# Performance work log

Measured on AMD Instinct MI355X. Metric: run time of the kernel, lower is better.

## Reference

```python
import jax, jax.numpy as jnp
import numpy as np

B_, L_, D_, N_ = 2, 2048, 512, 64

def setup_inputs() -> dict:
    key = jax.random.key(0)
    ks = jax.random.split(key, 6)
    s = 1.0 / np.sqrt(D_)
    return {
        "x": jax.random.normal(ks[0], (B_, L_, D_), dtype=jnp.float32),
        "W1": jax.random.normal(ks[1], (D_, D_), dtype=jnp.float32) * s,
        "b1": jnp.zeros((D_,), dtype=jnp.float32),
        "W2": jax.random.normal(ks[2], (D_, N_), dtype=jnp.float32) * s,
        "b2": jnp.zeros((N_,), dtype=jnp.float32),
        "W3": jax.random.normal(ks[3], (D_, N_), dtype=jnp.float32) * s,
        "b3": jnp.zeros((N_,), dtype=jnp.float32),
        "A": jax.random.normal(ks[4], (D_, N_), dtype=jnp.float32) * (1.0 / np.sqrt(N_)),
    }

def reference(x, W1, b1, W2, b2, W3, b3, A):
    # Projections (faithful to fc2/fc3/fc1 in the torch module)
    B = x @ W2 + b2                                  # (b, l, n)
    C = x @ W3 + b3                                  # (b, l, n)
    delta = jax.nn.softplus(x @ W1 + b1)             # (b, l, d)
    # Discretization
    dB = jnp.einsum('bld,bln->bldn', delta, B)       # (b, l, d, n)
    dA = jnp.exp(jnp.einsum('bld,dn->bldn', delta, A))  # (b, l, d, n)
    # h is initialized to zeros in the original forward, so the dA*h term
    # contributes exactly zero; kept for faithfulness to the source math.
    h = dA * 0.0 + x[..., None] * dB                 # (b, l, d, n)
    y = jnp.einsum('bln,bldn->bld', C, h)            # (b, l, d)
    return y
```

## Files before the change

### kernel.cpp

```cpp
#include <hip/hip_runtime.h>
#include <math.h>

#define DDIM 512
#define MTOK 4096

typedef _Float16 f16;
typedef _Float16 f16x4 __attribute__((ext_vector_type(4)));
typedef _Float16 f16x8 __attribute__((ext_vector_type(8)));
typedef float f32x4 __attribute__((ext_vector_type(4)));

__device__ __forceinline__ float softplusf(float v) {
    return (v > 20.0f) ? v : log1pf(__expf(v));
}

__device__ __forceinline__ void async_load16(const void* g, void* l) {
    __builtin_amdgcn_global_load_lds(
        (const __attribute__((address_space(1))) void*)g,
        (__attribute__((address_space(3))) void*)l, 16, 0, 0);
}

__global__ __launch_bounds__(256) void prep_kernel(
    const float* __restrict__ x,  const float* __restrict__ W1,
    const float* __restrict__ W2, const float* __restrict__ W3,
    f16* __restrict__ xh, f16* __restrict__ w1t, f16* __restrict__ w23)
{
    const int tid = threadIdx.x;
    if (blockIdx.x < 2048) {
        size_t gid = ((size_t)blockIdx.x * 256 + tid) * 4;
        float4 v = *(const float4*)(x + gid);
        f16x4 h = {(f16)v.x, (f16)v.y, (f16)v.z, (f16)v.w};
        *(f16x4*)(xh + gid) = h;
        return;
    }
    __shared__ f16 lt[64][72];
    int b2 = blockIdx.x - 2048;
    const float* src; f16* dst; int srcRS;
    if (b2 < 64) {
        int kt = b2 >> 3, nt = b2 & 7;
        src = W1 + (size_t)(kt * 64) * DDIM + nt * 64; srcRS = DDIM;
        dst = w1t + (size_t)(nt * 64) * DDIM + kt * 64;
    } else if (b2 < 72) {
        int kt = b2 - 64;
        src = W2 + (size_t)(kt * 64) * 64; srcRS = 64;
        dst = w23 + kt * 64;
    } else {
        int kt = b2 - 72;
        src = W3 + (size_t)(kt * 64) * 64; srcRS = 64;
        dst = w23 + (size_t)64 * DDIM + kt * 64;
    }
    int r  = tid >> 2;
    int cg = tid & 3;
#pragma unroll
    for (int p = 0; p < 4; ++p) {
        float4 v = *(const float4*)(src + (size_t)r * srcRS + cg * 16 + p * 4);
        lt[cg * 16 + p * 4 + 0][r] = (f16)v.x;
        lt[cg * 16 + p * 4 + 1][r] = (f16)v.y;
        lt[cg * 16 + p * 4 + 2][r] = (f16)v.z;
        lt[cg * 16 + p * 4 + 3][r] = (f16)v.w;
    }
    __syncthreads();
    *(f16x8*)(dst + (size_t)r * DDIM + cg * 16)     = *(const f16x8*)&lt[r][cg * 16];
    *(f16x8*)(dst + (size_t)r * DDIM + cg * 16 + 8) = *(const f16x8*)&lt[r][cg * 16 + 8];
}

#define S_BUF 20480
__global__ __launch_bounds__(256) void s_kernel(
    const f16* __restrict__ xh, const f16* __restrict__ w23,
    const float* __restrict__ b2, const float* __restrict__ b3,
    float* __restrict__ s_out)
{
    __shared__ __align__(16) char smem[2 * S_BUF + 512];
    float* sred = (float*)(smem + 2 * S_BUF);

    const int tid  = threadIdx.x;
    const int wv   = tid >> 6;
    const int lane = tid & 63;
    const int q    = lane >> 4;
    const int l15  = lane & 15;
    const int tb   = blockIdx.x * 32;

    f32x4 acc[2][2];
#pragma unroll
    for (int m = 0; m < 2; ++m)
#pragma unroll
        for (int p = 0; p < 2; ++p) acc[m][p] = (f32x4){0.f, 0.f, 0.f, 0.f};

    auto issue = [&](int buf, int kc) {
#pragma unroll
        for (int j = 0; j < 5; ++j) {
            int id = wv * 5 + j;
            const f16* g; int off;
            if (id < 4) {
                int mt = id >> 1, kk = id & 1;
                g = xh + (size_t)(tb + mt * 16 + l15) * DDIM + kc + kk * 32 + q * 8;
                off = id * 1024;
            } else {
                int t = id - 4; int nt = t >> 1, kk = t & 1;
                g = w23 + (size_t)(nt * 16 + l15) * DDIM + kc + kk * 32 + q * 8;
                off = 4096 + t * 1024;
            }
            async_load16(g, smem + buf * S_BUF + off);
        }
    };

    issue(0, 0);
    for (int it = 0; it < 8; ++it) {
        __syncthreads();
        if (it + 1 < 8) issue((it + 1) & 1, (it + 1) * 64);
        const char* xb = smem + (it & 1) * S_BUF;
        const char* wb = xb + 4096;
#pragma unroll
        for (int kk = 0; kk < 2; ++kk) {
            f16x8 a0 = *(const f16x8*)(xb + (0 * 2 + kk) * 1024 + lane * 16);
            f16x8 a1 = *(const f16x8*)(xb + (1 * 2 + kk) * 1024 + lane * 16);
            f16x8 bB = *(const f16x8*)(wb + ((wv    ) * 2 + kk) * 1024 + lane * 16);
            f16x8 bC = *(const f16x8*)(wb + ((wv + 4) * 2 + kk) * 1024 + lane * 16);
            acc[0][0] = __builtin_amdgcn_mfma_f32_16x16x32_f16(a0, bB, acc[0][0], 0, 0, 0);
            acc[0][1] = __builtin_amdgcn_mfma_f32_16x16x32_f16(a0, bC, acc[0][1], 0, 0, 0);
            acc[1][0] = __builtin_amdgcn_mfma_f32_16x16x32_f16(a1, bB, acc[1][0], 0, 0, 0);
            acc[1][1] = __builtin_amdgcn_mfma_f32_16x16x32_f16(a1, bC, acc[1][1], 0, 0, 0);
        }
    }

    float b2v = b2[wv * 16 + l15];
    float b3v = b3[wv * 16 + l15];
#pragma unroll
    for (int m = 0; m < 2; ++m)
#pragma unroll
        for (int r = 0; r < 4; ++r) {
            float p = (acc[m][0][r] + b2v) * (acc[m][1][r] + b3v);
            p += __shfl_xor(p, 1); p += __shfl_xor(p, 2);
            p += __shfl_xor(p, 4); p += __shfl_xor(p, 8);
            if (l15 == 0) sred[wv * 32 + m * 16 + q * 4 + r] = p;
        }
    __syncthreads();
    if (tid < 32)
        s_out[tb + tid] = sred[tid] + sred[32 + tid] + sred[64 + tid] + sred[96 + tid];
}

#define Y_BUF 24576
__global__ __launch_bounds__(512) void y_kernel(
    const f16* __restrict__ xh, const f16* __restrict__ w1t,
    const float* __restrict__ b1, const float* __restrict__ s_in,
    float* __restrict__ y)
{
    __shared__ __align__(16) char smem[2 * Y_BUF];

    const int tid  = threadIdx.x;
    const int wv   = tid >> 6;
    const int lane = tid & 63;
    const int q    = lane >> 4;
    const int l15  = lane & 15;
    const int db   = blockIdx.x * 64;
    const int tb   = blockIdx.y * 128;

    f32x4 acc[4];
#pragma unroll
    for (int nt = 0; nt < 4; ++nt) acc[nt] = (f32x4){0.f, 0.f, 0.f, 0.f};

    auto issue = [&](int buf, int kc) {
#pragma unroll
        for (int j = 0; j < 3; ++j) {
            int id = wv * 3 + j;
            const f16* g; int off;
            if (id < 16) {
                int mt = id >> 1, kk = id & 1;
                g = xh + (size_t)(tb + mt * 16 + l15) * DDIM + kc + kk * 32 + q * 8;
                off = id * 1024;
            } else {
                int t = id - 16; int nt = t >> 1, kk = t & 1;
                g = w1t + (size_t)(db + nt * 16 + l15) * DDIM + kc + kk * 32 + q * 8;
                off = 16384 + t * 1024;
            }
            async_load16(g, smem + buf * Y_BUF + off);
        }
    };

    issue(0, 0);
    for (int it = 0; it < 8; ++it) {
        __syncthreads();
        if (it + 1 < 8) issue((it + 1) & 1, (it + 1) * 64);
        const char* xb = smem + (it & 1) * Y_BUF;
        const char* wb = xb + 16384;
#pragma unroll
        for (int kk = 0; kk < 2; ++kk) {
            f16x8 a = *(const f16x8*)(xb + (wv * 2 + kk) * 1024 + lane * 16);
#pragma unroll
            for (int nt = 0; nt < 4; ++nt) {
                f16x8 b = *(const f16x8*)(wb + (nt * 2 + kk) * 1024 + lane * 16);
                acc[nt] = __builtin_amdgcn_mfma_f32_16x16x32_f16(a, b, acc[nt], 0, 0, 0);
            }
        }
    }

    float b1v[4];
#pragma unroll
    for (int nt = 0; nt < 4; ++nt) b1v[nt] = b1[db + nt * 16 + l15];
#pragma unroll
    for (int r = 0; r < 4; ++r) {
        int token = tb + wv * 16 + q * 4 + r;
        float st = s_in[token];
#pragma unroll
        for (int nt = 0; nt < 4; ++nt) {
            int d = db + nt * 16 + l15;
            float xv = (float)xh[(size_t)token * DDIM + d];
            y[(size_t)token * DDIM + d] = xv * softplusf(acc[nt][r] + b1v[nt]) * st;
        }
    }
}

extern "C" void kernel_launch(void* const* d_in, const int* in_sizes, int n_in,
                              void* d_out, int out_size, void* d_ws, size_t ws_size,
                              hipStream_t stream)
{
    (void)n_in; (void)out_size; (void)ws_size; (void)in_sizes;
    const float* x  = (const float*)d_in[0];
    const float* W1 = (const float*)d_in[1];
    const float* b1 = (const float*)d_in[2];
    const float* W2 = (const float*)d_in[3];
    const float* b2 = (const float*)d_in[4];
    const float* W3 = (const float*)d_in[5];
    const float* b3 = (const float*)d_in[6];
    float* y = (float*)d_out;

    char* ws  = (char*)d_ws;
    f16* xh   = (f16*)(ws);
    f16* w1t  = (f16*)(ws + (4 << 20));
    f16* w23  = (f16*)(ws + (4 << 20) + (512 << 10));
    float* sv = (float*)(ws + (5 << 20));

    prep_kernel<<<2048 + 80, 256, 0, stream>>>(x, W1, W2, W3, xh, w1t, w23);
    s_kernel<<<MTOK / 32, 256, 0, stream>>>(xh, w23, b2, b3, sv);
    y_kernel<<<dim3(DDIM / 64, MTOK / 128), 512, 0, stream>>>(xh, w1t, b1, sv, y);
}
```

Baseline: 102.2 us.

## Pre-swizzle fp16 operands into MFMA fragment layout for contiguous async loads

The prep kernel now writes x, W1^T and W2/W3 in a tiled fragment-major layout, where each 16x32 MFMA operand tile is a contiguous 1KB chunk. The s and y kernels can then issue fully contiguous 16-byte async LDS loads instead of strided row gathers. The s kernel now handles 16 tokens per block, giving it twice as many blocks. The y epilogue reads x in fp32 directly instead of the fp16 copy. Prep does more shared-memory work and uses fewer, larger blocks, which may lower its parallelism.

```diff
diff --git a/kernel.cpp b/kernel.cpp
--- a/kernel.cpp
+++ b/kernel.cpp
@@ -24,52 +24,70 @@
     const float* __restrict__ W2, const float* __restrict__ W3,
     f16* __restrict__ xh, f16* __restrict__ w1t, f16* __restrict__ w23)
 {
-    const int tid = threadIdx.x;
-    if (blockIdx.x < 2048) {
-        size_t gid = ((size_t)blockIdx.x * 256 + tid) * 4;
-        float4 v = *(const float4*)(x + gid);
-        f16x4 h = {(f16)v.x, (f16)v.y, (f16)v.z, (f16)v.w};
-        *(f16x4*)(xh + gid) = h;
+    __shared__ __align__(16) f16 lt[32][520];
+    const int tid  = threadIdx.x;
+    const int bid  = blockIdx.x;
+    const int wv   = tid >> 6;
+    const int lane = tid & 63;
+    const int q    = lane >> 4;
+    const int l15  = lane & 15;
+
+    if (bid < 256) {
+        const int mt  = bid;
+        const int row = tid >> 4;
+        const int cg  = tid & 15;
+        const float* xr = x + (size_t)(mt * 16 + row) * DDIM;
+#pragma unroll
+        for (int i = 0; i < 8; ++i) {
+            int col = cg * 4 + i * 64;
+            float4 v = *(const float4*)(xr + col);
+            f16x4 h = {(f16)v.x, (f16)v.y, (f16)v.z, (f16)v.w};
+            *(f16x4*)&lt[row][col] = h;
+        }
+        __syncthreads();
+#pragma unroll
+        for (int j = 0; j < 4; ++j) {
+            int kt = wv * 4 + j;
+            f16x8 vv = *(const f16x8*)&lt[l15][kt * 32 + q * 8];
+            *(f16x8*)(xh + (size_t)(mt * 16 + kt) * 512 + lane * 8) = vv;
+        }
         return;
     }
-    __shared__ f16 lt[64][72];
-    int b2 = blockIdx.x - 2048;
-    const float* src; f16* dst; int srcRS;
-    if (b2 < 64) {
-        int kt = b2 >> 3, nt = b2 & 7;
-        src = W1 + (size_t)(kt * 64) * DDIM + nt * 64; srcRS = DDIM;
-        dst = w1t + (size_t)(nt * 64) * DDIM + kt * 64;
-    } else if (b2 < 72) {
-        int kt = b2 - 64;
-        src = W2 + (size_t)(kt * 64) * 64; srcRS = 64;
-        dst = w23 + kt * 64;
-    } else {
-        int kt = b2 - 72;
-        src = W3 + (size_t)(kt * 64) * 64; srcRS = 64;
-        dst = w23 + (size_t)64 * DDIM + kt * 64;
-    }
-    int r  = tid >> 2;
-    int cg = tid & 3;
-#pragma unroll
-    for (int p = 0; p < 4; ++p) {
-        float4 v = *(const float4*)(src + (size_t)r * srcRS + cg * 16 + p * 4);
-        lt[cg * 16 + p * 4 + 0][r] = (f16)v.x;
-        lt[cg * 16 + p * 4 + 1][r] = (f16)v.y;
-        lt[cg * 16 + p * 4 + 2][r] = (f16)v.z;
-        lt[cg * 16 + p * 4 + 3][r] = (f16)v.w;
+    int wb = bid - 256;
+    const float* src; int srcRS, col0; f16* dst;
+    if (wb < 16)      { src = W1; srcRS = DDIM; col0 = wb * 32;
+                        dst = w1t + (size_t)wb * 2 * 16 * 512; }
+    else if (wb < 18) { src = W2; srcRS = 64;  col0 = (wb - 16) * 32;
+                        dst = w23 + (size_t)(wb - 16) * 2 * 16 * 512; }
+    else              { src = W3; srcRS = 64;  col0 = (wb - 18) * 32;
+                        dst = w23 + (size_t)(4 + (wb - 18) * 2) * 16 * 512; }
+#pragma unroll
+    for (int i = 0; i < 16; ++i) {
+        int f  = tid + 256 * i;
+        int k  = f >> 3;
+        int c4 = (f & 7) * 4;
+        float4 v = *(const float4*)(src + (size_t)k * srcRS + col0 + c4);
+        lt[c4 + 0][k] = (f16)v.x; lt[c4 + 1][k] = (f16)v.y;
+        lt[c4 + 2][k] = (f16)v.z; lt[c4 + 3][k] = (f16)v.w;
     }
     __syncthreads();
-    *(f16x8*)(dst + (size_t)r * DDIM + cg * 16)     = *(const f16x8*)&lt[r][cg * 16];
-    *(f16x8*)(dst + (size_t)r * DDIM + cg * 16 + 8) = *(const f16x8*)&lt[r][cg * 16 + 8];
-}
-
-#define S_BUF 20480
+#pragma unroll
+    for (int j = 0; j < 8; ++j) {
+        int s   = wv * 8 + j;
+        int ntL = s >> 4;
+        int kt  = s & 15;
+        f16x8 vv = *(const f16x8*)&lt[ntL * 16 + l15][kt * 32 + q * 8];
+        *(f16x8*)(dst + (size_t)(ntL * 16 + kt) * 512 + lane * 8) = vv;
+    }
+}
+
+#define S_BUF 18432
 __global__ __launch_bounds__(256) void s_kernel(
     const f16* __restrict__ xh, const f16* __restrict__ w23,
     const float* __restrict__ b2, const float* __restrict__ b3,
     float* __restrict__ s_out)
 {
-    __shared__ __align__(16) char smem[2 * S_BUF + 512];
+    __shared__ __align__(16) char smem[2 * S_BUF + 256];
     float* sred = (float*)(smem + 2 * S_BUF);
 
     const int tid  = threadIdx.x;
@@ -77,27 +95,27 @@
     const int lane = tid & 63;
     const int q    = lane >> 4;
     const int l15  = lane & 15;
-    const int tb   = blockIdx.x * 32;
-
-    f32x4 acc[2][2];
-#pragma unroll
-    for (int m = 0; m < 2; ++m)
-#pragma unroll
-        for (int p = 0; p < 2; ++p) acc[m][p] = (f32x4){0.f, 0.f, 0.f, 0.f};
-
-    auto issue = [&](int buf, int kc) {
+    const int mtG  = blockIdx.x;
+    const int tb   = mtG * 16;
+
+    f32x4 acc[2];
+    acc[0] = (f32x4){0.f, 0.f, 0.f, 0.f};
+    acc[1] = (f32x4){0.f, 0.f, 0.f, 0.f};
+
+    auto issue = [&](int buf, int it) {
+        int kt0 = it * 2;
 #pragma unroll
         for (int j = 0; j < 5; ++j) {
-            int id = wv * 5 + j;
+            int id = wv + 4 * j;
+            if (id >= 18) break;
             const f16* g; int off;
-            if (id < 4) {
-                int mt = id >> 1, kk = id & 1;
-                g = xh + (size_t)(tb + mt * 16 + l15) * DDIM + kc + kk * 32 + q * 8;
+            if (id < 2) {
+                g   = xh + (size_t)(mtG * 16 + kt0 + id) * 512 + lane * 8;
                 off = id * 1024;
             } else {
-                int t = id - 4; int nt = t >> 1, kk = t & 1;
-                g = w23 + (size_t)(nt * 16 + l15) * DDIM + kc + kk * 32 + q * 8;
-                off = 4096 + t * 1024;
+                int t = id - 2, nt = t >> 1, kk = t & 1;
+                g   = w23 + (size_t)(nt * 16 + kt0 + kk) * 512 + lane * 8;
+                off = 2048 + t * 1024;
             }
             async_load16(g, smem + buf * S_BUF + off);
         }
@@ -106,43 +124,38 @@
     issue(0, 0);
     for (int it = 0; it < 8; ++it) {
         __syncthreads();
-        if (it + 1 < 8) issue((it + 1) & 1, (it + 1) * 64);
+        if (it + 1 < 8) issue((it + 1) & 1, it + 1);
         const char* xb = smem + (it & 1) * S_BUF;
-        const char* wb = xb + 4096;
+        const char* wb = xb + 2048;
 #pragma unroll
         for (int kk = 0; kk < 2; ++kk) {
-            f16x8 a0 = *(const f16x8*)(xb + (0 * 2 + kk) * 1024 + lane * 16);
-            f16x8 a1 = *(const f16x8*)(xb + (1 * 2 + kk) * 1024 + lane * 16);
-            f16x8 bB = *(const f16x8*)(wb + ((wv    ) * 2 + kk) * 1024 + lane * 16);
-            f16x8 bC = *(const f16x8*)(wb + ((wv + 4) * 2 + kk) * 1024 + lane * 16);
-            acc[0][0] = __builtin_amdgcn_mfma_f32_16x16x32_f16(a0, bB, acc[0][0], 0, 0, 0);
-            acc[0][1] = __builtin_amdgcn_mfma_f32_16x16x32_f16(a0, bC, acc[0][1], 0, 0, 0);
-            acc[1][0] = __builtin_amdgcn_mfma_f32_16x16x32_f16(a1, bB, acc[1][0], 0, 0, 0);
-            acc[1][1] = __builtin_amdgcn_mfma_f32_16x16x32_f16(a1, bC, acc[1][1], 0, 0, 0);
+            f16x8 a  = *(const f16x8*)(xb + kk * 1024 + lane * 16);
+            f16x8 bB = *(const f16x8*)(wb + ((wv * 2 + kk)) * 1024 + lane * 16);
+            f16x8 bC = *(const f16x8*)(wb + (((4 + wv) * 2 + kk)) * 1024 + lane * 16);
+            acc[0] = __builtin_amdgcn_mfma_f32_16x16x32_f16(a, bB, acc[0], 0, 0, 0);
+            acc[1] = __builtin_amdgcn_mfma_f32_16x16x32_f16(a, bC, acc[1], 0, 0, 0);
         }
     }
 
     float b2v = b2[wv * 16 + l15];
     float b3v = b3[wv * 16 + l15];
 #pragma unroll
-    for (int m = 0; m < 2; ++m)
-#pragma unroll
-        for (int r = 0; r < 4; ++r) {
-            float p = (acc[m][0][r] + b2v) * (acc[m][1][r] + b3v);
-            p += __shfl_xor(p, 1); p += __shfl_xor(p, 2);
-            p += __shfl_xor(p, 4); p += __shfl_xor(p, 8);
-            if (l15 == 0) sred[wv * 32 + m * 16 + q * 4 + r] = p;
-        }
+    for (int r = 0; r < 4; ++r) {
+        float p = (acc[0][r] + b2v) * (acc[1][r] + b3v);
+        p += __shfl_xor(p, 1); p += __shfl_xor(p, 2);
+        p += __shfl_xor(p, 4); p += __shfl_xor(p, 8);
+        if (l15 == 0) sred[wv * 16 + q * 4 + r] = p;
+    }
     __syncthreads();
-    if (tid < 32)
-        s_out[tb + tid] = sred[tid] + sred[32 + tid] + sred[64 + tid] + sred[96 + tid];
+    if (tid < 16)
+        s_out[tb + tid] = sred[tid] + sred[16 + tid] + sred[32 + tid] + sred[48 + tid];
 }
 
 #define Y_BUF 24576
 __global__ __launch_bounds__(512) void y_kernel(
     const f16* __restrict__ xh, const f16* __restrict__ w1t,
-    const float* __restrict__ b1, const float* __restrict__ s_in,
-    float* __restrict__ y)
+    const float* __restrict__ x, const float* __restrict__ b1,
+    const float* __restrict__ s_in, float* __restrict__ y)
 {
     __shared__ __align__(16) char smem[2 * Y_BUF];
 
@@ -152,24 +165,27 @@
     const int q    = lane >> 4;
     const int l15  = lane & 15;
     const int db   = blockIdx.x * 64;
+    const int ntG  = blockIdx.x * 4;
     const int tb   = blockIdx.y * 128;
+    const int mtG  = blockIdx.y * 8;
 
     f32x4 acc[4];
 #pragma unroll
     for (int nt = 0; nt < 4; ++nt) acc[nt] = (f32x4){0.f, 0.f, 0.f, 0.f};
 
-    auto issue = [&](int buf, int kc) {
+    auto issue = [&](int buf, int it) {
+        int kt0 = it * 2;
 #pragma unroll
         for (int j = 0; j < 3; ++j) {
             int id = wv * 3 + j;
             const f16* g; int off;
             if (id < 16) {
                 int mt = id >> 1, kk = id & 1;
-                g = xh + (size_t)(tb + mt * 16 + l15) * DDIM + kc + kk * 32 + q * 8;
+                g   = xh + (size_t)((mtG + mt) * 16 + kt0 + kk) * 512 + lane * 8;
                 off = id * 1024;
             } else {
-                int t = id - 16; int nt = t >> 1, kk = t & 1;
-                g = w1t + (size_t)(db + nt * 16 + l15) * DDIM + kc + kk * 32 + q * 8;
+                int t = id - 16, nt = t >> 1, kk = t & 1;
+                g   = w1t + (size_t)((ntG + nt) * 16 + kt0 + kk) * 512 + lane * 8;
                 off = 16384 + t * 1024;
             }
             async_load16(g, smem + buf * Y_BUF + off);
@@ -179,7 +195,7 @@
     issue(0, 0);
     for (int it = 0; it < 8; ++it) {
         __syncthreads();
-        if (it + 1 < 8) issue((it + 1) & 1, (it + 1) * 64);
+        if (it + 1 < 8) issue((it + 1) & 1, it + 1);
         const char* xb = smem + (it & 1) * Y_BUF;
         const char* wb = xb + 16384;
 #pragma unroll
@@ -203,7 +219,7 @@
 #pragma unroll
         for (int nt = 0; nt < 4; ++nt) {
             int d = db + nt * 16 + l15;
-            float xv = (float)xh[(size_t)token * DDIM + d];
+            float xv = x[(size_t)token * DDIM + d];
             y[(size_t)token * DDIM + d] = xv * softplusf(acc[nt][r] + b1v[nt]) * st;
         }
     }
@@ -229,7 +245,7 @@
     f16* w23  = (f16*)(ws + (4 << 20) + (512 << 10));
     float* sv = (float*)(ws + (5 << 20));
 
-    prep_kernel<<<2048 + 80, 256, 0, stream>>>(x, W1, W2, W3, xh, w1t, w23);
-    s_kernel<<<MTOK / 32, 256, 0, stream>>>(xh, w23, b2, b3, sv);
-    y_kernel<<<dim3(DDIM / 64, MTOK / 128), 512, 0, stream>>>(xh, w1t, b1, sv, y);
-}
+    prep_kernel<<<276, 256, 0, stream>>>(x, W1, W2, W3, xh, w1t, w23);
+    s_kernel<<<MTOK / 16, 256, 0, stream>>>(xh, w23, b2, b3, sv);
+    y_kernel<<<dim3(DDIM / 64, MTOK / 128), 512, 0, stream>>>(xh, w1t, x, b1, sv, y);
+}
```

Measured after the change: 97.60 us. 4.5% less time.
